# Kernel optimization log

Hardware: AMD Instinct MI355X
Metric: run time of the kernel (lower is better)

## Reference

```python
import jax, jax.numpy as jnp
import numpy as np

B, N, S = 8, 8192, 64          # batch, media tokens, latent tokens
DIM, HEADS, DIM_HEAD = 512, 8, 64
INNER = HEADS * DIM_HEAD       # 512
PATCH = 16
SLICE = PATCH * PATCH          # 256
SCALE = DIM_HEAD ** -0.5
EPS = 1e-5


def _layernorm(x, g, b):
    mu = x.mean(axis=-1, keepdims=True)
    var = ((x - mu) ** 2).mean(axis=-1, keepdims=True)
    return (x - mu) * jax.lax.rsqrt(var + EPS) * g + b


def setup_inputs() -> dict:
    key = jax.random.key(0)
    ks = jax.random.split(key, 8)
    x = jax.random.normal(ks[0], (B, N, DIM), dtype=jnp.float32)
    latents = jax.random.normal(ks[1], (B, S, DIM), dtype=jnp.float32)
    indices = jax.random.randint(ks[2], (B,), 0, 32)
    w = lambda k, shp: jax.random.normal(k, shp, dtype=jnp.float32) * 0.02
    return {
        "x": x, "latents": latents, "indices": indices,
        "g_m": jnp.ones((DIM,), jnp.float32), "b_m": jnp.zeros((DIM,), jnp.float32),
        "g_l": jnp.ones((DIM,), jnp.float32), "b_l": jnp.zeros((DIM,), jnp.float32),
        "Wq": w(ks[3], (DIM, INNER)), "bq": jnp.zeros((INNER,), jnp.float32),
        "Wkv": w(ks[4], (DIM, 2 * INNER)), "bkv": jnp.zeros((2 * INNER,), jnp.float32),
        "Wo": w(ks[5], (INNER, DIM)), "bo": jnp.zeros((DIM,), jnp.float32),
    }


def reference(x, latents, indices, g_m, b_m, g_l, b_l, Wq, bq, Wkv, bkv, Wo, bo):
    b, n, _ = x.shape
    s = latents.shape[1]
    t = n + s
    xn = _layernorm(x, g_m, b_m)
    ln = _layernorm(latents, g_l, b_l)

    q = ln @ Wq + bq                              # [b, s, inner]
    kv = jnp.concatenate([xn, ln], axis=1) @ Wkv + bkv  # [b, t, 2*inner]
    k, v = jnp.split(kv, 2, axis=-1)

    def heads(z):  # b n (h d) -> b h n d
        return z.reshape(b, -1, HEADS, DIM_HEAD).transpose(0, 2, 1, 3)

    q, k, v = heads(q) * SCALE, heads(k), heads(v)

    sim = jnp.einsum("bhid,bhjd->bhij", q, k)     # [b, h, s, t]
    # media key j is visible iff j < indices[i]*SLICE; latents (j >= n) always visible
    j = jnp.arange(t)
    allowed = (j[None, :] < indices[:, None] * SLICE) | (j[None, :] >= n)  # [b, t]
    sim = jnp.where(allowed[:, None, None, :], sim, -jnp.inf)

    attn = jax.nn.softmax(sim, axis=-1)
    out = jnp.einsum("bhij,bhjd->bhid", attn, v)  # [b, h, s, d]
    out = out.transpose(0, 2, 1, 3).reshape(b, s, INNER)
    return out @ Wo + bo
```

## Files before the change

### kernel.cpp

```cpp
#include <hip/hip_runtime.h>


typedef unsigned short u16;
typedef __attribute__((ext_vector_type(8))) short bf16x8;
typedef __attribute__((ext_vector_type(4))) float f32x4;

__device__ __forceinline__ float b2f(u16 u) {
    union { unsigned u; float f; } v; v.u = ((unsigned)u) << 16; return v.f;
}
__device__ __forceinline__ u16 f2b(float f) {
    union { float f; unsigned u; } v; v.f = f; return (u16)(v.u >> 16);
}
__device__ __forceinline__ float ld(const void* p, size_t o, int bf) {
    return bf ? b2f(((const u16*)p)[o]) : ((const float*)p)[o];
}
__device__ __forceinline__ void ld8(const void* p, size_t o, int bf, float* out) {
    if (bf) {
        const ushort4* q = (const ushort4*)((const u16*)p + o);
        ushort4 u0 = q[0], u1 = q[1];
        out[0] = b2f(u0.x); out[1] = b2f(u0.y); out[2] = b2f(u0.z); out[3] = b2f(u0.w);
        out[4] = b2f(u1.x); out[5] = b2f(u1.y); out[6] = b2f(u1.z); out[7] = b2f(u1.w);
    } else {
        const float4* q = (const float4*)((const float*)p + o);
        float4 f0 = q[0], f1 = q[1];
        out[0] = f0.x; out[1] = f0.y; out[2] = f0.z; out[3] = f0.w;
        out[4] = f1.x; out[5] = f1.y; out[6] = f1.z; out[7] = f1.w;
    }
}

__global__ void k_report(float* __restrict__ out, float val) {
    out[(size_t)blockIdx.x * 256 + threadIdx.x] = val;
}

__global__ __launch_bounds__(256) void k_prep(const void* __restrict__ bq, const void* __restrict__ bkv,
        const void* __restrict__ bo, const void* __restrict__ g_m, const void* __restrict__ b_m,
        const void* __restrict__ g_l, const void* __restrict__ b_l, int* __restrict__ flag,
        float* __restrict__ bias_f, float* __restrict__ gb_f, float* __restrict__ zbase) {
    int blk = blockIdx.x, t = threadIdx.x;
    if (blk >= 16) {
        zbase[(size_t)(blk - 16) * 256 + t] = 0.f;
        return;
    }
    int bf = (((const u16*)g_m)[0] == 0x3F80) ? 1 : 0;
    if (blk == 0 && t == 0) *flag = bf;
    int u = blk * 256 + t;
    if (u < 512)       bias_f[u] = ld(bq, u, bf);
    else if (u < 1536) bias_f[u] = ld(bkv, u - 512, bf);
    else if (u < 2048) bias_f[u] = ld(bo, u - 1536, bf);
    else if (u < 2560) gb_f[u - 2048] = ld(g_m, u - 2048, bf);
    else if (u < 3072) gb_f[u - 2048] = ld(b_m, u - 2560, bf);
    else if (u < 3584) gb_f[u - 2048] = ld(g_l, u - 3072, bf);
    else               gb_f[u - 2048] = ld(b_l, u - 3584, bf);
}

__global__ __launch_bounds__(256) void k_muln(const void* __restrict__ x, const void* __restrict__ lat,
        const int* __restrict__ flag, float* __restrict__ murs) {
    int b = blockIdx.y, wv = threadIdx.x >> 6, lane = threadIdx.x & 63;
    int r = blockIdx.x * 4 + wv, bf = *flag;
    size_t ro = (r < 8192) ? ((size_t)b * 8192 + r) * 512 : ((size_t)b * 64 + (r - 8192)) * 512;
    const void* src = (r < 8192) ? x : lat;
    float v[8];
    ld8(src, ro + lane * 8, bf, v);
    float s = 0.f, q = 0.f;
#pragma unroll
    for (int e = 0; e < 8; e++) { s += v[e]; q += v[e] * v[e]; }
    for (int m = 32; m; m >>= 1) { s += __shfl_xor(s, m, 64); q += __shfl_xor(q, m, 64); }
    float mu = s * (1.f / 512.f);
    float var = q * (1.f / 512.f) - mu * mu;
    float rs = rsqrtf(var + 1e-5f);
    if (lane == 0) {
        murs[((size_t)b * 8256 + r) * 2] = mu;
        murs[((size_t)b * 8256 + r) * 2 + 1] = rs;
    }
}

__global__ __launch_bounds__(256) void k_lnlat(const void* __restrict__ lat, const int* __restrict__ flag,
        const float* __restrict__ murs, const float* __restrict__ gb_f, float* __restrict__ lnL) {
    int bf = *flag;
    int u = blockIdx.x * 256 + threadIdx.x;
    int g = u >> 6, c0 = (u & 63) * 8;
    int b = g >> 6, i = g & 63;
    float mu = murs[((size_t)b * 8256 + 8192 + i) * 2];
    float rs = murs[((size_t)b * 8256 + 8192 + i) * 2 + 1];
    float v[8];
    ld8(lat, ((size_t)b * 64 + i) * 512 + c0, bf, v);
    float o[8];
#pragma unroll
    for (int e = 0; e < 8; e++)
        o[e] = (v[e] - mu) * rs * gb_f[1024 + c0 + e] + gb_f[1536 + c0 + e];
    *(float4*)&lnL[(size_t)g * 512 + c0]     = make_float4(o[0], o[1], o[2], o[3]);
    *(float4*)&lnL[(size_t)g * 512 + c0 + 4] = make_float4(o[4], o[5], o[6], o[7]);
}

__global__ __launch_bounds__(256) void k_gemm512(const float* __restrict__ A, const void* __restrict__ W,
        const int* __restrict__ flag, const float* __restrict__ bias_f, int bias_off, float scale,
        const float* __restrict__ lden, float* __restrict__ C) {
    int ry = blockIdx.x, cx = blockIdx.y, t = threadIdx.x, bf = *flag;
    __shared__ float As[32][68];
    __shared__ float Bs[32][68];
    int arow = t >> 2, ak0 = (t & 3) * 8;
    int bk = t >> 3, bn0 = (t & 7) * 8;
    int tm = t >> 4, tn = t & 15;
    int g8 = (ry * 64 + arow) * 8;
    float acc[4][4];
#pragma unroll
    for (int i = 0; i < 4; i++)
#pragma unroll
        for (int j = 0; j < 4; j++) acc[i][j] = 0.f;
    float sa[8], sb[8];
    const float* ap = A + (size_t)(ry * 64 + arow) * 512;
    *(float4*)&sa[0] = *(const float4*)(ap + ak0);
    *(float4*)&sa[4] = *(const float4*)(ap + ak0 + 4);
    ld8(W, (size_t)bk * 512 + cx * 64 + bn0, bf, sb);
    float inv = 1.f;
    for (int ch = 0; ch < 16; ch++) {
        int kk = ch * 32;
        if (ch) __syncthreads();
        if (lden && (ch & 1) == 0) inv = 1.f / lden[g8 + (ch >> 1)];
#pragma unroll
        for (int e = 0; e < 8; e++) As[ak0 + e][arow] = sa[e] * inv;
        *(float4*)&Bs[bk][bn0]     = make_float4(sb[0], sb[1], sb[2], sb[3]);
        *(float4*)&Bs[bk][bn0 + 4] = make_float4(sb[4], sb[5], sb[6], sb[7]);
        __syncthreads();
        if (ch < 15) {
            int kn = kk + 32;
            *(float4*)&sa[0] = *(const float4*)(ap + kn + ak0);
            *(float4*)&sa[4] = *(const float4*)(ap + kn + ak0 + 4);
            ld8(W, (size_t)(kn + bk) * 512 + cx * 64 + bn0, bf, sb);
        }
#pragma unroll 8
        for (int k = 0; k < 32; k++) {
            float4 a4 = *(const float4*)&As[k][tm * 4];
            float4 b4 = *(const float4*)&Bs[k][tn * 4];
            float aa[4] = {a4.x, a4.y, a4.z, a4.w};
            float bb[4] = {b4.x, b4.y, b4.z, b4.w};
#pragma unroll
            for (int i = 0; i < 4; i++)
#pragma unroll
                for (int j = 0; j < 4; j++) acc[i][j] += aa[i] * bb[j];
        }
    }
#pragma unroll
    for (int r = 0; r < 4; r++) {
        int n0 = cx * 64 + tn * 4;
        float4 v;
        v.x = (acc[r][0] + bias_f[bias_off + n0 + 0]) * scale;
        v.y = (acc[r][1] + bias_f[bias_off + n0 + 1]) * scale;
        v.z = (acc[r][2] + bias_f[bias_off + n0 + 2]) * scale;
        v.w = (acc[r][3] + bias_f[bias_off + n0 + 3]) * scale;
        *(float4*)&C[(size_t)(ry * 64 + tm * 4 + r) * 512 + n0] = v;
    }
}

__global__ __launch_bounds__(256) void k_kv5(int b0, size_t kvstr,
        const void* __restrict__ x, const void* __restrict__ lat,
        const void* __restrict__ Wkv, const int* __restrict__ idx, const int* __restrict__ flag,
        const float* __restrict__ murs, const float* __restrict__ gb_f, const float* __restrict__ bias_f,
        float* __restrict__ Kb, float* __restrict__ Vb) {
    int zb = blockIdx.x >> 9;
    int bb = b0 + zb;
    int L = blockIdx.x & 511;
    int ry = (L & 7) + ((L >> 6) << 3);
    int cx = (L >> 3) & 7;
    if (ry > 62) return;
    int mv = idx[bb] * 256;
    if (ry < 62 && ry * 128 >= mv) return;
    int bf = *flag, t = threadIdx.x;
    int w = t >> 6, l = t & 63;

    __shared__ u16 Ah[128 * 40], Al[128 * 40];
    __shared__ u16 Bh[128 * 40], Bl[128 * 40];
    __shared__ float gS[512], bS[512];

    int go = (ry == 62) ? 1024 : 0;
    for (int u = t; u < 512; u += 256) { gS[u] = gb_f[go + u]; bS[u] = gb_f[go + 512 + u]; }

    int am = t >> 1, ac0 = (t & 1) * 16;
    int ar = ry * 128 + am;
    const void* asrc; size_t aro; int li = 0;
    if (ar < 7936) { asrc = x; aro = ((size_t)bb * 8192 + ar) * 512; }
    else { li = ar - 7936; if (li > 63) li = 63; asrc = lat; aro = ((size_t)bb * 64 + li) * 512; }
    int mr = (ar < 7936) ? ar : (8192 + li);
    float mu = murs[((size_t)bb * 8256 + mr) * 2];
    float rs = murs[((size_t)bb * 8256 + mr) * 2 + 1];

    int kp = (t >> 4) * 2, cn0 = (t & 15) * 8;
    int ncol0 = cx * 128;

    const bool splitB = (bf == 0);

    f32x4 acc[2][8];
#pragma unroll
    for (int i = 0; i < 2; i++)
#pragma unroll
        for (int j = 0; j < 8; j++) acc[i][j] = (f32x4){0.f, 0.f, 0.f, 0.f};

    float sa[16], sb0[8], sb1[8];
    ld8(asrc, aro + ac0, bf, sa); ld8(asrc, aro + ac0 + 8, bf, sa + 8);
    ld8(Wkv, (size_t)kp * 1024 + ncol0 + cn0, bf, sb0);
    ld8(Wkv, (size_t)(kp + 1) * 1024 + ncol0 + cn0, bf, sb1);
    __syncthreads();

    for (int ch = 0; ch < 16; ch++) {
        int kk = ch * 32;
        if (ch) __syncthreads();
#pragma unroll
        for (int e2 = 0; e2 < 8; e2++) {
            int kl = ac0 + e2 * 2;
            float a0 = (sa[e2 * 2]     - mu) * rs * gS[kk + kl]     + bS[kk + kl];
            float a1 = (sa[e2 * 2 + 1] - mu) * rs * gS[kk + kl + 1] + bS[kk + kl + 1];
            u16 h0 = f2b(a0), h1 = f2b(a1);
            u16 lo0 = f2b(a0 - b2f(h0)), lo1 = f2b(a1 - b2f(h1));
            *(ushort2*)&Ah[am * 40 + kl] = make_ushort2(h0, h1);
            *(ushort2*)&Al[am * 40 + kl] = make_ushort2(lo0, lo1);
        }
#pragma unroll
        for (int e = 0; e < 8; e++) {
            u16 h0 = f2b(sb0[e]), h1 = f2b(sb1[e]);
            *(ushort2*)&Bh[(cn0 + e) * 40 + kp] = make_ushort2(h0, h1);
            if (splitB) {
                u16 lo0 = f2b(sb0[e] - b2f(h0)), lo1 = f2b(sb1[e] - b2f(h1));
                *(ushort2*)&Bl[(cn0 + e) * 40 + kp] = make_ushort2(lo0, lo1);
            }
        }
        __syncthreads();
        if (ch < 15) {
            int kn = kk + 32;
            ld8(asrc, aro + kn + ac0, bf, sa); ld8(asrc, aro + kn + ac0 + 8, bf, sa + 8);
            ld8(Wkv, (size_t)(kn + kp) * 1024 + ncol0 + cn0, bf, sb0);
            ld8(Wkv, (size_t)(kn + kp + 1) * 1024 + ncol0 + cn0, bf, sb1);
        }
        int g8 = (l >> 4) * 8;
        bf16x8 ah0 = *(const bf16x8*)&Ah[(w * 32 +      (l & 15)) * 40 + g8];
        bf16x8 ah1 = *(const bf16x8*)&Ah[(w * 32 + 16 + (l & 15)) * 40 + g8];
        bf16x8 al0 = *(const bf16x8*)&Al[(w * 32 +      (l & 15)) * 40 + g8];
        bf16x8 al1 = *(const bf16x8*)&Al[(w * 32 + 16 + (l & 15)) * 40 + g8];
#pragma unroll
        for (int ct = 0; ct < 8; ct++) {
            bf16x8 bh = *(const bf16x8*)&Bh[(ct * 16 + (l & 15)) * 40 + g8];
            acc[0][ct] = __builtin_amdgcn_mfma_f32_16x16x32_bf16(ah0, bh, acc[0][ct], 0, 0, 0);
            acc[1][ct] = __builtin_amdgcn_mfma_f32_16x16x32_bf16(ah1, bh, acc[1][ct], 0, 0, 0);
            acc[0][ct] = __builtin_amdgcn_mfma_f32_16x16x32_bf16(al0, bh, acc[0][ct], 0, 0, 0);
            acc[1][ct] = __builtin_amdgcn_mfma_f32_16x16x32_bf16(al1, bh, acc[1][ct], 0, 0, 0);
            if (splitB) {
                bf16x8 bl = *(const bf16x8*)&Bl[(ct * 16 + (l & 15)) * 40 + g8];
                acc[0][ct] = __builtin_amdgcn_mfma_f32_16x16x32_bf16(ah0, bl, acc[0][ct], 0, 0, 0);
                acc[1][ct] = __builtin_amdgcn_mfma_f32_16x16x32_bf16(ah1, bl, acc[1][ct], 0, 0, 0);
            }
        }
    }
    float* dst; int coff;
    if (ncol0 < 512) { dst = Kb; coff = ncol0; } else { dst = Vb; coff = ncol0 - 512; }
    dst += (size_t)zb * kvstr;
#pragma unroll
    for (int rt = 0; rt < 2; rt++) {
#pragma unroll
        for (int ct = 0; ct < 8; ct++) {
            int row = ry * 128 + w * 32 + rt * 16 + (l >> 4) * 4;
            int cloc = ct * 16 + (l & 15);
            float bias = bias_f[512 + ncol0 + cloc];
#pragma unroll
            for (int r = 0; r < 4; r++)
                dst[(size_t)(row + r) * 512 + coff + cloc] = acc[rt][ct][r] + bias;
        }
    }
}

__global__ __launch_bounds__(256) void k_attn_f(int b0, size_t kvstr, const int* __restrict__ idx,
        const float* __restrict__ qf, const float* __restrict__ Kb, const float* __restrict__ Vb,
        float* __restrict__ ao, float* __restrict__ Lden) {
    int h = blockIdx.x, c = blockIdx.y, zb = blockIdx.z, t = threadIdx.x;
    int bb = b0 + zb;
    int mv = idx[bb] * 256;
    int row0, nsub;
    if (c == 31) { row0 = 7936; nsub = 1; }
    else { row0 = c * 256; nsub = 4; if (row0 >= mv) return; }
    const float* Kp = Kb + (size_t)zb * kvstr;
    const float* Vp = Vb + (size_t)zb * kvstr;
    int tq = t >> 4, tj = t & 15;
    __shared__ float Qt[64][68];
    __shared__ float Kt[64][68];
    __shared__ float Vs[64][68];
    __shared__ float Pt[64][68];
    const float* qbase = qf + (size_t)bb * 64 * 512 + h * 64;
#pragma unroll
    for (int it = 0; it < 4; it++) {
        int id = t + it * 256;
        int q = id >> 4, d0 = (id & 15) * 4;
        float4 v = *(const float4*)(qbase + (size_t)q * 512 + d0);
        Qt[d0 + 0][q] = v.x; Qt[d0 + 1][q] = v.y; Qt[d0 + 2][q] = v.z; Qt[d0 + 3][q] = v.w;
    }
    float oacc[4][4] = {{0.f}};
    float lp[4] = {0.f, 0.f, 0.f, 0.f};
    for (int st = 0; st < nsub; st++) {
        int jb = row0 + st * 64;
        __syncthreads();
#pragma unroll
        for (int it = 0; it < 4; it++) {
            int id = t + it * 256;
            int j = id >> 4, d0 = (id & 15) * 4;
            float4 k4 = *(const float4*)(Kp + (size_t)(jb + j) * 512 + h * 64 + d0);
            Kt[d0 + 0][j] = k4.x; Kt[d0 + 1][j] = k4.y; Kt[d0 + 2][j] = k4.z; Kt[d0 + 3][j] = k4.w;
            *(float4*)&Vs[j][d0] = *(const float4*)(Vp + (size_t)(jb + j) * 512 + h * 64 + d0);
        }
        __syncthreads();
        float s[4][4] = {{0.f}};
#pragma unroll 4
        for (int d = 0; d < 64; d++) {
            float4 q4 = *(const float4*)&Qt[d][tq * 4];
            float4 k4 = *(const float4*)&Kt[d][tj * 4];
            float qa[4] = {q4.x, q4.y, q4.z, q4.w};
            float ka[4] = {k4.x, k4.y, k4.z, k4.w};
#pragma unroll
            for (int r = 0; r < 4; r++)
#pragma unroll
                for (int cc = 0; cc < 4; cc++) s[r][cc] += qa[r] * ka[cc];
        }
#pragma unroll
        for (int cc = 0; cc < 4; cc++) {
            float4 pw;
            pw.x = __expf(s[0][cc]); pw.y = __expf(s[1][cc]);
            pw.z = __expf(s[2][cc]); pw.w = __expf(s[3][cc]);
            *(float4*)&Pt[tj * 4 + cc][tq * 4] = pw;
        }
        __syncthreads();
#pragma unroll 4
        for (int j = 0; j < 64; j++) {
            float4 p4 = *(const float4*)&Pt[j][tq * 4];
            float4 v4 = *(const float4*)&Vs[j][tj * 4];
            float pa[4] = {p4.x, p4.y, p4.z, p4.w};
            float va[4] = {v4.x, v4.y, v4.z, v4.w};
            if (tj == 0) { lp[0] += pa[0]; lp[1] += pa[1]; lp[2] += pa[2]; lp[3] += pa[3]; }
#pragma unroll
            for (int r = 0; r < 4; r++)
#pragma unroll
                for (int cc = 0; cc < 4; cc++) oacc[r][cc] += pa[r] * va[cc];
        }
    }
    float* abase = ao + ((size_t)bb * 64 + tq * 4) * 512 + h * 64 + tj * 4;
#pragma unroll
    for (int r = 0; r < 4; r++)
#pragma unroll
        for (int cc = 0; cc < 4; cc++)
            atomicAdd(abase + (size_t)r * 512 + cc, oacc[r][cc]);
    if (tj == 0) {
#pragma unroll
        for (int r = 0; r < 4; r++)
            atomicAdd(&Lden[((size_t)bb * 64 + tq * 4 + r) * 8 + h], lp[r]);
    }
}

extern "C" void kernel_launch(void* const* d_in, const int* in_sizes, int n_in,
                              void* d_out, int out_size, void* d_ws, size_t ws_size,
                              hipStream_t stream) {
    (void)in_sizes; (void)n_in;
    const void* x   = d_in[0];
    const void* lat = d_in[1];
    const int*  idx = (const int*)d_in[2];
    float* out = (float*)d_out;

    const size_t KV1B       = 16515072;
    const size_t NEED_SMALL = 2658560 + 2 * KV1B;
    const size_t NEED_BIG   = 2658560 + 16 * KV1B;
    if (ws_size < NEED_SMALL || d_ws == nullptr) {
        float val = 100.0f + (float)(ws_size >> 20);
        hipLaunchKernelGGL(k_report, dim3((out_size + 255) / 256), dim3(256), 0, stream, out, val);
        return;
    }
    const bool big = (ws_size >= NEED_BIG);
    char* ws = (char*)d_ws;
    int*   flag   = (int*)ws;
    float* bias_f = (float*)(ws + 256);
    float* gb_f   = (float*)(ws + 8448);
    float* murs   = (float*)(ws + 16640);
    float* qf     = (float*)(ws + 545024);
    float* ao     = (float*)(ws + 1593600);
    float* Lden   = (float*)(ws + 2642176);
    float* Kb     = (float*)(ws + 2658560);
    float* Vb     = big ? (float*)(ws + 2658560 + 8 * KV1B)
                        : (float*)(ws + 2658560 + KV1B);
    float* lnL    = Kb;
    const size_t kvstr = big ? (KV1B / 4) : 0;

    hipLaunchKernelGGL(k_prep, dim3(1056), dim3(256), 0, stream,
                       d_in[8], d_in[10], d_in[12], d_in[3], d_in[4], d_in[5], d_in[6],
                       flag, bias_f, gb_f, ao);
    hipLaunchKernelGGL(k_muln, dim3(2064, 8), dim3(256), 0, stream, x, lat, flag, murs);
    hipLaunchKernelGGL(k_lnlat, dim3(128), dim3(256), 0, stream, lat, flag, murs, gb_f, lnL);
    hipLaunchKernelGGL(k_gemm512, dim3(8, 8), dim3(256), 0, stream,
                       lnL, d_in[7], flag, bias_f, 0, 0.125f, (const float*)nullptr, qf);
    if (big) {
        hipLaunchKernelGGL(k_kv5, dim3(8 * 512), dim3(256), 0, stream,
                           0, kvstr, x, lat, d_in[9], idx, flag, murs, gb_f, bias_f, Kb, Vb);
        hipLaunchKernelGGL(k_attn_f, dim3(8, 32, 8), dim3(256), 0, stream,
                           0, kvstr, idx, qf, Kb, Vb, ao, Lden);
    } else {
        for (int b = 0; b < 8; b++) {
            hipLaunchKernelGGL(k_kv5, dim3(512), dim3(256), 0, stream,
                               b, kvstr, x, lat, d_in[9], idx, flag, murs, gb_f, bias_f, Kb, Vb);
            hipLaunchKernelGGL(k_attn_f, dim3(8, 32, 1), dim3(256), 0, stream,
                               b, kvstr, idx, qf, Kb, Vb, ao, Lden);
        }
    }
    hipLaunchKernelGGL(k_gemm512, dim3(8, 8), dim3(256), 0, stream,
                       ao, d_in[11], flag, bias_f, 1536, 1.0f, Lden, out);
}
```

Before: 579.9 us.

## Pre-swizzle Wkv into MFMA fragment layout and drop LDS staging in KV GEMM

```diff
diff --git a/kernel.cpp b/kernel.cpp
--- a/kernel.cpp
+++ b/kernel.cpp
@@ -53,6 +53,26 @@
     else               gb_f[u - 2048] = ld(b_l, u - 3584, bf);
 }
 
+__global__ __launch_bounds__(256) void k_wsw(const void* __restrict__ Wkv, const int* __restrict__ flag,
+        u16* __restrict__ wh, u16* __restrict__ wl) {
+    int t = threadIdx.x, bf = *flag;
+    int g = blockIdx.x * 4 + (t >> 6), l = t & 63;
+    int kc = g >> 6, cb = g & 63;
+    int kbase = kc * 32 + (l >> 4) * 8, col = cb * 16 + (l & 15);
+    u16 h[8], o[8];
+#pragma unroll
+    for (int j = 0; j < 8; j++) {
+        float v = ld(Wkv, (size_t)(kbase + j) * 1024 + col, bf);
+        h[j] = f2b(v);
+        o[j] = f2b(v - b2f(h[j]));
+    }
+    size_t off = ((size_t)g * 64 + l) * 8;
+    *(ushort4*)&wh[off]     = make_ushort4(h[0], h[1], h[2], h[3]);
+    *(ushort4*)&wh[off + 4] = make_ushort4(h[4], h[5], h[6], h[7]);
+    *(ushort4*)&wl[off]     = make_ushort4(o[0], o[1], o[2], o[3]);
+    *(ushort4*)&wl[off + 4] = make_ushort4(o[4], o[5], o[6], o[7]);
+}
+
 __global__ __launch_bounds__(256) void k_muln(const void* __restrict__ x, const void* __restrict__ lat,
         const int* __restrict__ flag, float* __restrict__ murs) {
     int b = blockIdx.y, wv = threadIdx.x >> 6, lane = threadIdx.x & 63;
@@ -152,11 +172,12 @@
     }
 }
 
-__global__ __launch_bounds__(256) void k_kv5(int b0, size_t kvstr,
+__global__ __launch_bounds__(256) void k_kv6(int b0, size_t kvstr,
         const void* __restrict__ x, const void* __restrict__ lat,
-        const void* __restrict__ Wkv, const int* __restrict__ idx, const int* __restrict__ flag,
-        const float* __restrict__ murs, const float* __restrict__ gb_f, const float* __restrict__ bias_f,
-        float* __restrict__ Kb, float* __restrict__ Vb) {
+        const u16* __restrict__ wh, const u16* __restrict__ wl,
+        const int* __restrict__ idx, const int* __restrict__ flag,
+        const float* __restrict__ murs, const float* __restrict__ gb_f,
+        const float* __restrict__ bias_f, float* __restrict__ Kb, float* __restrict__ Vb) {
     int zb = blockIdx.x >> 9;
     int bb = b0 + zb;
     int L = blockIdx.x & 511;
@@ -167,83 +188,73 @@
     if (ry < 62 && ry * 128 >= mv) return;
     int bf = *flag, t = threadIdx.x;
     int w = t >> 6, l = t & 63;
-
-    __shared__ u16 Ah[128 * 40], Al[128 * 40];
-    __shared__ u16 Bh[128 * 40], Bl[128 * 40];
-    __shared__ float gS[512], bS[512];
-
+    int lr = l & 15, g8 = (l >> 4) * 8;
     int go = (ry == 62) ? 1024 : 0;
-    for (int u = t; u < 512; u += 256) { gS[u] = gb_f[go + u]; bS[u] = gb_f[go + 512 + u]; }
-
-    int am = t >> 1, ac0 = (t & 1) * 16;
-    int ar = ry * 128 + am;
-    const void* asrc; size_t aro; int li = 0;
-    if (ar < 7936) { asrc = x; aro = ((size_t)bb * 8192 + ar) * 512; }
-    else { li = ar - 7936; if (li > 63) li = 63; asrc = lat; aro = ((size_t)bb * 64 + li) * 512; }
-    int mr = (ar < 7936) ? ar : (8192 + li);
-    float mu = murs[((size_t)bb * 8256 + mr) * 2];
-    float rs = murs[((size_t)bb * 8256 + mr) * 2 + 1];
-
-    int kp = (t >> 4) * 2, cn0 = (t & 15) * 8;
+
+    int r0 = ry * 128 + w * 32 + lr;
+    int r1 = r0 + 16;
+    const void* asrc; size_t aro0, aro1; int mr0, mr1;
+    if (ry < 62) {
+        asrc = x;
+        aro0 = ((size_t)bb * 8192 + r0) * 512; aro1 = ((size_t)bb * 8192 + r1) * 512;
+        mr0 = r0; mr1 = r1;
+    } else {
+        int li0 = r0 - 7936; if (li0 > 63) li0 = 63;
+        int li1 = r1 - 7936; if (li1 > 63) li1 = 63;
+        asrc = lat;
+        aro0 = ((size_t)bb * 64 + li0) * 512; aro1 = ((size_t)bb * 64 + li1) * 512;
+        mr0 = 8192 + li0; mr1 = 8192 + li1;
+    }
+    float mu0 = murs[((size_t)bb * 8256 + mr0) * 2];
+    float rs0 = murs[((size_t)bb * 8256 + mr0) * 2 + 1];
+    float mu1 = murs[((size_t)bb * 8256 + mr1) * 2];
+    float rs1 = murs[((size_t)bb * 8256 + mr1) * 2 + 1];
+
+    const bool splitB = (bf == 0);
     int ncol0 = cx * 128;
 
-    const bool splitB = (bf == 0);
-
     f32x4 acc[2][8];
 #pragma unroll
     for (int i = 0; i < 2; i++)
 #pragma unroll
         for (int j = 0; j < 8; j++) acc[i][j] = (f32x4){0.f, 0.f, 0.f, 0.f};
 
-    float sa[16], sb0[8], sb1[8];
-    ld8(asrc, aro + ac0, bf, sa); ld8(asrc, aro + ac0 + 8, bf, sa + 8);
-    ld8(Wkv, (size_t)kp * 1024 + ncol0 + cn0, bf, sb0);
-    ld8(Wkv, (size_t)(kp + 1) * 1024 + ncol0 + cn0, bf, sb1);
-    __syncthreads();
+    float sa0[8], sa1[8];
+    ld8(asrc, aro0 + g8, bf, sa0);
+    ld8(asrc, aro1 + g8, bf, sa1);
 
     for (int ch = 0; ch < 16; ch++) {
         int kk = ch * 32;
-        if (ch) __syncthreads();
-#pragma unroll
-        for (int e2 = 0; e2 < 8; e2++) {
-            int kl = ac0 + e2 * 2;
-            float a0 = (sa[e2 * 2]     - mu) * rs * gS[kk + kl]     + bS[kk + kl];
-            float a1 = (sa[e2 * 2 + 1] - mu) * rs * gS[kk + kl + 1] + bS[kk + kl + 1];
+        float gg[8], bb_[8];
+        *(float4*)&gg[0]  = *(const float4*)&gb_f[go + kk + g8];
+        *(float4*)&gg[4]  = *(const float4*)&gb_f[go + kk + g8 + 4];
+        *(float4*)&bb_[0] = *(const float4*)&gb_f[go + 512 + kk + g8];
+        *(float4*)&bb_[4] = *(const float4*)&gb_f[go + 512 + kk + g8 + 4];
+        bf16x8 ah0, ah1, al0, al1;
+#pragma unroll
+        for (int j = 0; j < 8; j++) {
+            float a0 = (sa0[j] - mu0) * rs0 * gg[j] + bb_[j];
+            float a1 = (sa1[j] - mu1) * rs1 * gg[j] + bb_[j];
             u16 h0 = f2b(a0), h1 = f2b(a1);
-            u16 lo0 = f2b(a0 - b2f(h0)), lo1 = f2b(a1 - b2f(h1));
-            *(ushort2*)&Ah[am * 40 + kl] = make_ushort2(h0, h1);
-            *(ushort2*)&Al[am * 40 + kl] = make_ushort2(lo0, lo1);
-        }
-#pragma unroll
-        for (int e = 0; e < 8; e++) {
-            u16 h0 = f2b(sb0[e]), h1 = f2b(sb1[e]);
-            *(ushort2*)&Bh[(cn0 + e) * 40 + kp] = make_ushort2(h0, h1);
-            if (splitB) {
-                u16 lo0 = f2b(sb0[e] - b2f(h0)), lo1 = f2b(sb1[e] - b2f(h1));
-                *(ushort2*)&Bl[(cn0 + e) * 40 + kp] = make_ushort2(lo0, lo1);
-            }
-        }
-        __syncthreads();
+            u16 o0 = f2b(a0 - b2f(h0)), o1 = f2b(a1 - b2f(h1));
+            ah0[j] = (short)h0; al0[j] = (short)o0;
+            ah1[j] = (short)h1; al1[j] = (short)o1;
+        }
         if (ch < 15) {
-            int kn = kk + 32;
-            ld8(asrc, aro + kn + ac0, bf, sa); ld8(asrc, aro + kn + ac0 + 8, bf, sa + 8);
-            ld8(Wkv, (size_t)(kn + kp) * 1024 + ncol0 + cn0, bf, sb0);
-            ld8(Wkv, (size_t)(kn + kp + 1) * 1024 + ncol0 + cn0, bf, sb1);
-        }
-        int g8 = (l >> 4) * 8;
-        bf16x8 ah0 = *(const bf16x8*)&Ah[(w * 32 +      (l & 15)) * 40 + g8];
-        bf16x8 ah1 = *(const bf16x8*)&Ah[(w * 32 + 16 + (l & 15)) * 40 + g8];
-        bf16x8 al0 = *(const bf16x8*)&Al[(w * 32 +      (l & 15)) * 40 + g8];
-        bf16x8 al1 = *(const bf16x8*)&Al[(w * 32 + 16 + (l & 15)) * 40 + g8];
+            ld8(asrc, aro0 + kk + 32 + g8, bf, sa0);
+            ld8(asrc, aro1 + kk + 32 + g8, bf, sa1);
+        }
+        const u16* whp = wh + (((size_t)ch * 64 + cx * 8) * 64 + l) * 8;
+        const u16* wlp = wl + (((size_t)ch * 64 + cx * 8) * 64 + l) * 8;
 #pragma unroll
         for (int ct = 0; ct < 8; ct++) {
-            bf16x8 bh = *(const bf16x8*)&Bh[(ct * 16 + (l & 15)) * 40 + g8];
+            bf16x8 bh = *(const bf16x8*)(whp + (size_t)ct * 512);
             acc[0][ct] = __builtin_amdgcn_mfma_f32_16x16x32_bf16(ah0, bh, acc[0][ct], 0, 0, 0);
             acc[1][ct] = __builtin_amdgcn_mfma_f32_16x16x32_bf16(ah1, bh, acc[1][ct], 0, 0, 0);
             acc[0][ct] = __builtin_amdgcn_mfma_f32_16x16x32_bf16(al0, bh, acc[0][ct], 0, 0, 0);
             acc[1][ct] = __builtin_amdgcn_mfma_f32_16x16x32_bf16(al1, bh, acc[1][ct], 0, 0, 0);
             if (splitB) {
-                bf16x8 bl = *(const bf16x8*)&Bl[(ct * 16 + (l & 15)) * 40 + g8];
+                bf16x8 bl = *(const bf16x8*)(wlp + (size_t)ct * 512);
                 acc[0][ct] = __builtin_amdgcn_mfma_f32_16x16x32_bf16(ah0, bl, acc[0][ct], 0, 0, 0);
                 acc[1][ct] = __builtin_amdgcn_mfma_f32_16x16x32_bf16(ah1, bl, acc[1][ct], 0, 0, 0);
             }
@@ -360,14 +371,16 @@
     float* out = (float*)d_out;
 
     const size_t KV1B       = 16515072;
-    const size_t NEED_SMALL = 2658560 + 2 * KV1B;
-    const size_t NEED_BIG   = 2658560 + 16 * KV1B;
+    const size_t WSWB       = 2097152;
+    const size_t NEED_SMALL = 2658560 + 2 * KV1B + 2 * WSWB;
+    const size_t NEED_BIG   = 2658560 + 16 * KV1B + 2 * WSWB;
     if (ws_size < NEED_SMALL || d_ws == nullptr) {
         float val = 100.0f + (float)(ws_size >> 20);
         hipLaunchKernelGGL(k_report, dim3((out_size + 255) / 256), dim3(256), 0, stream, out, val);
         return;
     }
     const bool big = (ws_size >= NEED_BIG);
+    const int nb = big ? 8 : 1;
     char* ws = (char*)d_ws;
     int*   flag   = (int*)ws;
     float* bias_f = (float*)(ws + 256);
@@ -377,27 +390,29 @@
     float* ao     = (float*)(ws + 1593600);
     float* Lden   = (float*)(ws + 2642176);
     float* Kb     = (float*)(ws + 2658560);
-    float* Vb     = big ? (float*)(ws + 2658560 + 8 * KV1B)
-                        : (float*)(ws + 2658560 + KV1B);
+    float* Vb     = (float*)(ws + 2658560 + (size_t)nb * KV1B);
+    u16*   wh     = (u16*)(ws + 2658560 + (size_t)2 * nb * KV1B);
+    u16*   wl     = (u16*)(ws + 2658560 + (size_t)2 * nb * KV1B + WSWB);
     float* lnL    = Kb;
     const size_t kvstr = big ? (KV1B / 4) : 0;
 
     hipLaunchKernelGGL(k_prep, dim3(1056), dim3(256), 0, stream,
                        d_in[8], d_in[10], d_in[12], d_in[3], d_in[4], d_in[5], d_in[6],
                        flag, bias_f, gb_f, ao);
+    hipLaunchKernelGGL(k_wsw, dim3(256), dim3(256), 0, stream, d_in[9], flag, wh, wl);
     hipLaunchKernelGGL(k_muln, dim3(2064, 8), dim3(256), 0, stream, x, lat, flag, murs);
     hipLaunchKernelGGL(k_lnlat, dim3(128), dim3(256), 0, stream, lat, flag, murs, gb_f, lnL);
     hipLaunchKernelGGL(k_gemm512, dim3(8, 8), dim3(256), 0, stream,
                        lnL, d_in[7], flag, bias_f, 0, 0.125f, (const float*)nullptr, qf);
     if (big) {
-        hipLaunchKernelGGL(k_kv5, dim3(8 * 512), dim3(256), 0, stream,
-                           0, kvstr, x, lat, d_in[9], idx, flag, murs, gb_f, bias_f, Kb, Vb);
+        hipLaunchKernelGGL(k_kv6, dim3(8 * 512), dim3(256), 0, stream,
+                           0, kvstr, x, lat, wh, wl, idx, flag, murs, gb_f, bias_f, Kb, Vb);
         hipLaunchKernelGGL(k_attn_f, dim3(8, 32, 8), dim3(256), 0, stream,
                            0, kvstr, idx, qf, Kb, Vb, ao, Lden);
     } else {
         for (int b = 0; b < 8; b++) {
-            hipLaunchKernelGGL(k_kv5, dim3(512), dim3(256), 0, stream,
-                               b, kvstr, x, lat, d_in[9], idx, flag, murs, gb_f, bias_f, Kb, Vb);
+            hipLaunchKernelGGL(k_kv6, dim3(512), dim3(256), 0, stream,
+                               b, kvstr, x, lat, wh, wl, idx, flag, murs, gb_f, bias_f, Kb, Vb);
             hipLaunchKernelGGL(k_attn_f, dim3(8, 32, 1), dim3(256), 0, stream,
                                b, kvstr, idx, qf, Kb, Vb, ao, Lden);
         }
```

Result: slower. 699.8 us (+20.7%).
